# Optimization experiments

Hardware: AMD Instinct MI355X
Metric: run time of the kernel (lower is better)

The kernel has to match this reference:

```python
import jax, jax.numpy as jnp
import numpy as np

D_MODEL = 1024
N_HEADS = 16
D_HEAD = D_MODEL // N_HEADS  # 64
M = int(round(D_HEAD * np.log(D_HEAD)))  # 266 random features, per source
KERNEL_EPS = 1e-4


def setup_inputs() -> dict:
    key = jax.random.key(0)
    ks = jax.random.split(key, 12)
    B, L = 2, 2048
    sc = 1.0 / np.sqrt(D_MODEL)
    return {
        "query": jax.random.normal(ks[0], (B, L, D_MODEL), jnp.float32),
        "key_": jax.random.normal(ks[1], (B, L, D_MODEL), jnp.float32),
        "value": jax.random.normal(ks[2], (B, L, D_MODEL), jnp.float32),
        "Wq": jax.random.normal(ks[3], (D_MODEL, D_MODEL), jnp.float32) * sc,
        "bq": jnp.zeros((D_MODEL,), jnp.float32),
        "Wk": jax.random.normal(ks[4], (D_MODEL, D_MODEL), jnp.float32) * sc,
        "bk": jnp.zeros((D_MODEL,), jnp.float32),
        "Wv": jax.random.normal(ks[5], (D_MODEL, D_MODEL), jnp.float32) * sc,
        "bv": jnp.zeros((D_MODEL,), jnp.float32),
        "Wo": jax.random.normal(ks[6], (D_MODEL, D_MODEL), jnp.float32) * sc,
        "bo": jnp.zeros((D_MODEL,), jnp.float32),
        "random_features": jax.random.normal(ks[7], (M, D_HEAD), jnp.float32),
    }


def _split_heads(x):
    # [B,L,d_model] -> [B,H,L,D]
    B, L, _ = x.shape
    return x.reshape(B, L, N_HEADS, D_HEAD).transpose(0, 2, 1, 3)


def _favor_projected(q, k, rf):
    # q,k: [B,H,L,D]; rf: [M,D]. Faithful to get_projected_queries_and_keys (kernel_type='exp').
    q = q / (D_MODEL ** 0.25)
    k = k / (D_MODEL ** 0.25)
    pq = jnp.einsum('bhld,md->bhlm', q, rf)
    pk = jnp.einsum('bhld,md->bhlm', k, rf)
    h_q = -0.5 * jnp.sum(q * q, axis=-1, keepdims=True)  # [B,H,L,1]
    h_k = -0.5 * jnp.sum(k * k, axis=-1, keepdims=True)
    q_stab = jnp.max(h_q, axis=-1, keepdims=True)  # == h_q (last dim is 1), as in source
    k_stab = jnp.max(h_k)  # global scalar, as in source
    q_ker = jnp.exp(h_q + (pq - q_stab))
    k_ker = jnp.exp(h_k + (pk - k_stab))
    c = M ** (-0.5)
    return c * (q_ker + KERNEL_EPS), c * (k_ker + KERNEL_EPS)


def _causal_favor(qp, kp, v):
    # qp,kp: [L,B,H,M]; v: [L,B,H,D]. Prefix-sum linear attention.
    # Denominator: q_prime[i] . cumsum(k_prime)[i]
    denom = jnp.einsum('lbhm,lbhm->lbh', qp, jnp.cumsum(kp, axis=0))

    # Numerator: recurrent scan carrying S = sum_j k'_j v_j^T  ([B,H,M,D])
    def step(S, inp):
        q_t, k_t, v_t = inp
        S = S + k_t[..., :, None] * v_t[..., None, :]
        out_t = jnp.einsum('bhmd,bhm->bhd', S, q_t)
        return S, out_t

    S0 = jnp.zeros(kp.shape[1:] + (v.shape[-1],), kp.dtype)
    _, num = jax.lax.scan(step, S0, (qp, kp, v))  # num: [L,B,H,D]
    return num / denom[..., None]


def reference(query, key_, value, Wq, bq, Wk, bk, Wv, bv, Wo, bo, random_features):
    B, L, _ = query.shape
    q = _split_heads(query @ Wq + bq)   # [B,H,L,D]
    k = _split_heads(key_ @ Wk + bk)
    v = _split_heads(value @ Wv + bv)
    q_prime, k_prime = _favor_projected(q, k, random_features)  # [B,H,L,M]
    # Causal path operates sequence-first: [L,B,H,*]
    qp = q_prime.transpose(2, 0, 1, 3)
    kp = k_prime.transpose(2, 0, 1, 3)
    vt = v.transpose(2, 0, 1, 3)
    out = _causal_favor(qp, kp, vt)               # [L,B,H,D]
    ctx = out.transpose(1, 0, 2, 3).reshape(B, L, D_MODEL)
    return ctx @ Wo + bo
```

## Files before the change

kernel.cpp:

```cpp
#include <hip/hip_runtime.h>
#include <hip/hip_bf16.h>

#define BATCH 2
#define SEQ 2048
#define DMODEL 1024
#define NH 16
#define HD 64
#define NRF 266
#define NRFP 288
#define SROW 320
#define CHK 128
#define NCH 16
#define NBH 32
#define NROWS 4096

constexpr float SCAL = 0.17677669529663687f;
constexpr float SCAL2 = 0.03125f;
constexpr float LN_CNORM = -2.7917480361965505f;
constexpr float CKEPS = 6.131393094576169e-6f;

typedef short bf16x8 __attribute__((ext_vector_type(8)));
typedef float f32x4 __attribute__((ext_vector_type(4)));

__device__ __forceinline__ short f2bs(float v) {
  __hip_bfloat16 h = __float2bfloat16(v);
  return *reinterpret_cast<short*>(&h);
}
__device__ __forceinline__ float bs2f(short s) {
  __hip_bfloat16 h;
  *reinterpret_cast<short*>(&h) = s;
  return __bfloat162float(h);
}
__device__ __forceinline__ void gload_lds16(const void* g, void* l) {
  __builtin_amdgcn_global_load_lds(
      (const __attribute__((address_space(1))) void*)g,
      (__attribute__((address_space(3))) void*)l, 16, 0, 0);
}
__device__ __forceinline__ unsigned f2ord(float f) {
  unsigned u = __float_as_uint(f);
  return (u & 0x80000000u) ? ~u : (u | 0x80000000u);
}
__device__ __forceinline__ float ord2f(unsigned e) {
  return (e & 0x80000000u) ? __uint_as_float(e & 0x7fffffffu)
                           : __uint_as_float(~e);
}

__global__ __launch_bounds__(256) void cvt3_kernel(const float* __restrict__ q,
                                                   const float* __restrict__ k,
                                                   const float* __restrict__ v,
                                                   short* __restrict__ out) {
  int z = blockIdx.y;
  const float* x = (z == 0) ? q : (z == 1) ? k : v;
  short* y = out + (size_t)z * NROWS * DMODEL;
  int i = (blockIdx.x * 256 + threadIdx.x) * 8;
  float4 a = *(const float4*)&x[i];
  float4 b = *(const float4*)&x[i + 4];
  bf16x8 o;
  o[0] = f2bs(a.x); o[1] = f2bs(a.y); o[2] = f2bs(a.z); o[3] = f2bs(a.w);
  o[4] = f2bs(b.x); o[5] = f2bs(b.y); o[6] = f2bs(b.z); o[7] = f2bs(b.w);
  *(bf16x8*)&y[i] = o;
}

__global__ __launch_bounds__(256) void rf_pad_bf16(const float* __restrict__ rf,
                                                   short* __restrict__ rfb,
                                                   unsigned* __restrict__ kord) {
  int idx = blockIdx.x * 256 + threadIdx.x;
  rfb[idx] = (idx < NRF * HD) ? f2bs(rf[idx] * SCAL) : (short)0;
  if (idx == 0) *kord = 0u;
}

__global__ __launch_bounds__(256) void transpose4_bf16(
    const float* __restrict__ Wq, const float* __restrict__ Wk,
    const float* __restrict__ Wv, const float* __restrict__ Wo,
    short* __restrict__ WtBase) {
  __shared__ float t[32][33];
  int z = blockIdx.z;
  const float* W = (z == 0) ? Wq : (z == 1) ? Wk : (z == 2) ? Wv : Wo;
  short* Wt = WtBase + (size_t)z * DMODEL * DMODEL;
  int k0 = blockIdx.y << 5, n0 = blockIdx.x << 5;
  int tx = threadIdx.x & 31, ty = threadIdx.x >> 5;
#pragma unroll
  for (int rr = 0; rr < 4; ++rr) {
    int r = ty + (rr << 3);
    t[r][tx] = W[(size_t)(k0 + r) * DMODEL + n0 + tx];
  }
  __syncthreads();
#pragma unroll
  for (int rr = 0; rr < 4; ++rr) {
    int r = ty + (rr << 3);
    Wt[(size_t)(n0 + r) * DMODEL + k0 + tx] = f2bs(t[tx][r]);
  }
}

template <bool OUTBF>
__device__ __forceinline__ void gemm_core128(const short* __restrict__ A,
                                             const short* __restrict__ Bt,
                                             const float* __restrict__ bias,
                                             void* __restrict__ C, int bm, int bn) {
  __shared__ short As[2][128 * 64];
  __shared__ short Bs[2][128 * 64];
  int tid = threadIdx.x;
  int lane = tid & 63, wid = tid >> 6;
  int wr = wid >> 1, wc = wid & 1;
  int cl = lane & 15, rq = lane >> 4;
  f32x4 acc[4][4];
#pragma unroll
  for (int m = 0; m < 4; ++m)
#pragma unroll
    for (int n = 0; n < 4; ++n) acc[m][n] = f32x4{0.f, 0.f, 0.f, 0.f};

  auto stage = [&](int buf, int k0) {
#pragma unroll
    for (int i = 0; i < 4; ++i) {
      int e = tid * 8 + i * 2048;
      int row = e >> 6;
      int k = (e & 63) ^ ((row & 7) << 3);
      gload_lds16(A + (size_t)(bm + row) * DMODEL + k0 + k,
                  &As[buf][wid * 512 + i * 2048]);
    }
#pragma unroll
    for (int i = 0; i < 4; ++i) {
      int e = tid * 8 + i * 2048;
      int row = e >> 6;
      int k = (e & 63) ^ ((row & 7) << 3);
      gload_lds16(Bt + (size_t)(bn + row) * DMODEL + k0 + k,
                  &Bs[buf][wid * 512 + i * 2048]);
    }
  };

  stage(0, 0);
#pragma unroll 2
  for (int t = 0; t < 16; ++t) {
    int cur = t & 1;
    if (t < 15) {
      stage(cur ^ 1, (t + 1) * 64);
      asm volatile("s_waitcnt vmcnt(8)" ::: "memory");
    } else {
      asm volatile("s_waitcnt vmcnt(0)" ::: "memory");
    }
    __builtin_amdgcn_s_barrier();
    asm volatile("" ::: "memory");
    const short* curA = &As[cur][0];
    const short* curB = &Bs[cur][0];
#pragma unroll
    for (int ks = 0; ks < 2; ++ks) {
      int kb = ks * 32 + (rq << 3);
      bf16x8 af[4], bfv[4];
#pragma unroll
      for (int mf = 0; mf < 4; ++mf) {
        int row = wr * 64 + mf * 16 + cl;
        af[mf] = *(const bf16x8*)&curA[row * 64 + (kb ^ ((row & 7) << 3))];
      }
#pragma unroll
      for (int nf = 0; nf < 4; ++nf) {
        int row = wc * 64 + nf * 16 + cl;
        bfv[nf] = *(const bf16x8*)&curB[row * 64 + (kb ^ ((row & 7) << 3))];
      }
#pragma unroll
      for (int mf = 0; mf < 4; ++mf)
#pragma unroll
        for (int nf = 0; nf < 4; ++nf)
          acc[mf][nf] = __builtin_amdgcn_mfma_f32_16x16x32_bf16(af[mf], bfv[nf],
                                                                acc[mf][nf], 0, 0, 0);
    }
    __builtin_amdgcn_s_barrier();
    asm volatile("" ::: "memory");
  }
  int rbase = bm + wr * 64 + (rq << 2);
  int cbase = bn + wc * 64 + cl;
#pragma unroll
  for (int nf = 0; nf < 4; ++nf) {
    int col = cbase + nf * 16;
    float bv = bias[col];
#pragma unroll
    for (int mf = 0; mf < 4; ++mf)
#pragma unroll
      for (int r = 0; r < 4; ++r) {
        int row = rbase + mf * 16 + r;
        float v = acc[mf][nf][r] + bv;
        if (OUTBF)
          ((short*)C)[(size_t)row * DMODEL + col] = f2bs(v);
        else
          ((float*)C)[(size_t)row * DMODEL + col] = v;
      }
  }
}

template <bool OUTBF>
__device__ __forceinline__ void gemm_core64(const short* __restrict__ A,
                                            const short* __restrict__ Bt,
                                            const float* __restrict__ bias,
                                            void* __restrict__ C, int bm, int bn) {
  __shared__ short As[2][128 * 64];
  __shared__ short Bs[2][64 * 64];
  int tid = threadIdx.x;
  int lane = tid & 63, wid = tid >> 6;
  int wr = wid >> 1, wc = wid & 1;
  f32x4 acc[4][2];
#pragma unroll
  for (int m = 0; m < 4; ++m)
#pragma unroll
    for (int n = 0; n < 2; ++n) acc[m][n] = f32x4{0.f, 0.f, 0.f, 0.f};

  auto stage = [&](int buf, int k0) {
#pragma unroll
    for (int i = 0; i < 4; ++i) {
      int e = tid * 8 + i * 2048;
      int row = e >> 6;
      int k = (e & 63) ^ ((row & 7) << 3);
      gload_lds16(A + (size_t)(bm + row) * DMODEL + k0 + k,
                  &As[buf][wid * 512 + i * 2048]);
    }
#pragma unroll
    for (int i = 0; i < 2; ++i) {
      int e = tid * 8 + i * 2048;
      int row = e >> 6;
      int k = (e & 63) ^ ((row & 7) << 3);
      gload_lds16(Bt + (size_t)(bn + row) * DMODEL + k0 + k,
                  &Bs[buf][wid * 512 + i * 2048]);
    }
  };

  stage(0, 0);
#pragma unroll 2
  for (int t = 0; t < 16; ++t) {
    int cur = t & 1;
    if (t < 15) {
      stage(cur ^ 1, (t + 1) * 64);
      asm volatile("s_waitcnt vmcnt(6)" ::: "memory");
    } else {
      asm volatile("s_waitcnt vmcnt(0)" ::: "memory");
    }
    __builtin_amdgcn_s_barrier();
    asm volatile("" ::: "memory");
    const short* curA = &As[cur][0];
    const short* curB = &Bs[cur][0];
#pragma unroll
    for (int ks = 0; ks < 2; ++ks) {
      int kb = ks * 32 + ((lane >> 4) << 3);
      bf16x8 af[4], bfv[2];
#pragma unroll
      for (int mf = 0; mf < 4; ++mf) {
        int row = wr * 64 + mf * 16 + (lane & 15);
        af[mf] = *(const bf16x8*)&curA[row * 64 + (kb ^ ((row & 7) << 3))];
      }
#pragma unroll
      for (int nf = 0; nf < 2; ++nf) {
        int row = wc * 32 + nf * 16 + (lane & 15);
        bfv[nf] = *(const bf16x8*)&curB[row * 64 + (kb ^ ((row & 7) << 3))];
      }
#pragma unroll
      for (int mf = 0; mf < 4; ++mf)
#pragma unroll
        for (int nf = 0; nf < 2; ++nf)
          acc[mf][nf] = __builtin_amdgcn_mfma_f32_16x16x32_bf16(af[mf], bfv[nf],
                                                                acc[mf][nf], 0, 0, 0);
    }
    __builtin_amdgcn_s_barrier();
    asm volatile("" ::: "memory");
  }
  int rbase = bm + wr * 64 + ((lane >> 4) << 2);
  int cbase = bn + wc * 32 + (lane & 15);
#pragma unroll
  for (int nf = 0; nf < 2; ++nf) {
    int col = cbase + nf * 16;
    float bv = bias[col];
#pragma unroll
    for (int mf = 0; mf < 4; ++mf)
#pragma unroll
      for (int r = 0; r < 4; ++r) {
        int row = rbase + mf * 16 + r;
        float v = acc[mf][nf][r] + bv;
        if (OUTBF)
          ((short*)C)[(size_t)row * DMODEL + col] = f2bs(v);
        else
          ((float*)C)[(size_t)row * DMODEL + col] = v;
      }
  }
}

__global__ __launch_bounds__(256) void gemm_qkv3(
    const short* __restrict__ Abase, const short* __restrict__ WtBase,
    const float* __restrict__ bq, const float* __restrict__ bk,
    const float* __restrict__ bv, short* __restrict__ OutBase) {
  int z = blockIdx.z;
  const short* A = Abase + (size_t)z * NROWS * DMODEL;
  const short* Bt = WtBase + (size_t)z * DMODEL * DMODEL;
  const float* bias = (z == 0) ? bq : (z == 1) ? bk : bv;
  short* C = OutBase + (size_t)z * NROWS * DMODEL;
  int bid = blockIdx.x + (blockIdx.y << 3);
  int swz = ((bid & 7) << 5) + (bid >> 3);
  int bn = (swz & 7) << 7;
  int bm = (swz >> 3) << 7;
  gemm_core128<true>(A, Bt, bias, C, bm, bn);
}

__global__ __launch_bounds__(256) void gemm_out(const short* __restrict__ A,
                                                const short* __restrict__ Bt,
                                                const float* __restrict__ bias,
                                                float* __restrict__ C) {
  int bid = blockIdx.x + (blockIdx.y << 4);
  int swz = ((bid & 7) << 6) + (bid >> 3);
  int bn = (swz & 15) << 6;
  int bm = (swz >> 4) << 7;
  gemm_core64<false>(A, Bt, bias, C, bm, bn);
}

__global__ __launch_bounds__(256) void hk_kernel(const short* __restrict__ Kb,
                                                 float* __restrict__ hkbuf,
                                                 unsigned* __restrict__ kord) {
  int tid = threadIdx.x;
  int rloc = tid >> 4, h = tid & 15;
  int n = blockIdx.x * 16 + rloc;
  const short* p = Kb + (size_t)n * DMODEL + h * HD;
  float ss = 0.f;
#pragma unroll
  for (int g = 0; g < 8; ++g) {
    bf16x8 v = *(const bf16x8*)(p + g * 8);
#pragma unroll
    for (int e = 0; e < 8; ++e) {
      float x = bs2f(v[e]);
      ss += x * x;
    }
  }
  float hkv = -0.5f * SCAL2 * ss;
  int b = n >> 11, l = n & (SEQ - 1);
  hkbuf[((size_t)(b * NH + h)) * SEQ + l] = hkv;
  __shared__ float red[256];
  red[tid] = hkv;
  __syncthreads();
  for (int s = 128; s > 0; s >>= 1) {
    if (tid < s) red[tid] = fmaxf(red[tid], red[tid + s]);
    __syncthreads();
  }
  if (tid == 0) atomicMax(kord, f2ord(red[0]));
}

__global__ __launch_bounds__(256, 1) void featmap_mfma(
    const short* __restrict__ Qproj, const short* __restrict__ Kproj,
    const short* __restrict__ rfb, const float* __restrict__ hkbuf,
    const unsigned* __restrict__ kord, short* __restrict__ Qp,
    short* __restrict__ Kp) {
  __shared__ short smem[26624];
  __shared__ float hks[128];
  short* As = smem;
  short* Bs = smem + 8192;
  int isK = blockIdx.z;
  const short* X = isK ? Kproj : Qproj;
  short* O = isK ? Kp : Qp;
  int bh = blockIdx.y, b = bh >> 4, h = bh & 15;
  int l0 = blockIdx.x << 7;
  int tid = threadIdx.x, lane = tid & 63, wid = tid >> 6;
  int cl = lane & 15, rq = lane >> 4;

#pragma unroll
  for (int i = 0; i < 4; ++i) {
    int e = tid * 8 + i * 2048;
    int row = e >> 6;
    int k = (e & 63) ^ ((row & 7) << 3);
    gload_lds16(X + ((size_t)b * SEQ + l0 + row) * DMODEL + h * HD + k,
                &As[wid * 512 + i * 2048]);
  }
#pragma unroll
  for (int i = 0; i < 9; ++i) {
    int e = tid * 8 + i * 2048;
    int row = e >> 6;
    int k = (e & 63) ^ ((row & 7) << 3);
    gload_lds16(rfb + row * HD + k, &Bs[wid * 512 + i * 2048]);
  }
  if (isK) {
    float ksv = ord2f(*kord);
    if (tid < 128)
      hks[tid] = hkbuf[(size_t)bh * SEQ + l0 + tid] - ksv + LN_CNORM;
  }
  __syncthreads();

  int i0 = wid * 32;
  f32x4 acc[2][18];
#pragma unroll
  for (int m = 0; m < 2; ++m)
#pragma unroll
    for (int n = 0; n < 18; ++n) acc[m][n] = f32x4{0.f, 0.f, 0.f, 0.f};
#pragma unroll
  for (int ks = 0; ks < 2; ++ks) {
    int kb = ks * 32 + (rq << 3);
    int swz = (cl & 7) << 3;
    bf16x8 af[2];
#pragma unroll
    for (int mf = 0; mf < 2; ++mf) {
      int row = i0 + mf * 16 + cl;
      af[mf] = *(const bf16x8*)&As[row * 64 + (kb ^ swz)];
    }
#pragma unroll
    for (int nf = 0; nf < 18; ++nf) {
      int brow = nf * 16 + cl;
      bf16x8 bv = *(const bf16x8*)&Bs[brow * 64 + (kb ^ swz)];
#pragma unroll
      for (int mf = 0; mf < 2; ++mf)
        acc[mf][nf] = __builtin_amdgcn_mfma_f32_16x16x32_bf16(af[mf], bv,
                                                              acc[mf][nf], 0, 0, 0);
    }
  }

  short* Ps = smem;
#pragma unroll
  for (int hf = 0; hf < 2; ++hf) {
    __syncthreads();
#pragma unroll
    for (int mf = 0; mf < 2; ++mf)
#pragma unroll
      for (int r = 0; r < 4; ++r) {
        int rl = i0 + mf * 16 + (rq << 2) + r;
        float addk = isK ? hks[rl] : LN_CNORM;
#pragma unroll
        for (int nf2 = 0; nf2 < 9; ++nf2) {
          int m = hf * 144 + nf2 * 16 + cl;
          float v = acc[mf][hf * 9 + nf2][r] + addk;
          float o = (m < NRF) ? (__expf(v) + CKEPS) : 0.f;
          Ps[rl * 152 + nf2 * 16 + cl] = f2bs(o);
        }
      }
    __syncthreads();
#pragma unroll
    for (int it = 0; it < 9; ++it) {
      int idx = tid + it * 256;
      int row = idx / 18, ch = idx - row * 18;
      bf16x8 val = *(const bf16x8*)&Ps[row * 152 + ch * 8];
      *(bf16x8*)&O[((size_t)bh * SEQ + l0 + row) * NRFP + hf * 144 + ch * 8] = val;
    }
  }
}

__global__ __launch_bounds__(256) void chunksum_mfma(
    const short* __restrict__ Kp, const short* __restrict__ Vb,
    short* __restrict__ Sct, float* __restrict__ ksum) {
  constexpr int ST = 70;
  __shared__ short KT[NRFP * ST];
  __shared__ short VT[HD * ST];
  int c = blockIdx.x, bh = blockIdx.y;
  int b = bh >> 4, h = bh & 15;
  int tid = threadIdx.x, lane = tid & 63, wv = tid >> 6;
  int cl = lane & 15, rq = lane >> 4;
  int irow = tid >> 2;
  int mq = tid & 3;
  size_t rowb = (size_t)bh * SEQ + (size_t)c * CHK;

  f32x4 acc[18];
#pragma unroll
  for (int m = 0; m < 18; ++m) acc[m] = f32x4{0.f, 0.f, 0.f, 0.f};
  float k1 = 0.f, k2 = 0.f;

  for (int hf = 0; hf < 2; ++hf) {
    __syncthreads();
    const short* Krow = Kp + (rowb + hf * 64 + irow) * NRFP;
#pragma unroll
    for (int cg = 0; cg < 9; ++cg) {
      int m0 = cg * 32 + mq * 8;
      bf16x8 v = *(const bf16x8*)(Krow + m0);
#pragma unroll
      for (int e = 0; e < 8; ++e) KT[(m0 + e) * ST + irow] = v[e];
    }
    const short* Vrow =
        Vb + ((size_t)b * SEQ + (size_t)c * CHK + hf * 64 + irow) * DMODEL + h * HD;
    {
      int d0 = mq * 16;
      bf16x8 v0 = *(const bf16x8*)(Vrow + d0);
      bf16x8 v1 = *(const bf16x8*)(Vrow + d0 + 8);
#pragma unroll
      for (int e = 0; e < 8; ++e) VT[(d0 + e) * ST + irow] = v0[e];
#pragma unroll
      for (int e = 0; e < 8; ++e) VT[(d0 + 8 + e) * ST + irow] = v1[e];
    }
    __syncthreads();
#pragma unroll
    for (int ks = 0; ks < 2; ++ks) {
      int kb = ks * 32 + rq * 8;
      bf16x8 bv = *(const bf16x8*)&VT[(wv * 16 + cl) * ST + kb];
#pragma unroll
      for (int mf = 0; mf < 18; ++mf) {
        bf16x8 av = *(const bf16x8*)&KT[(mf * 16 + cl) * ST + kb];
        acc[mf] = __builtin_amdgcn_mfma_f32_16x16x32_bf16(av, bv, acc[mf], 0, 0, 0);
      }
    }
    {
      const short* r1 = &KT[tid * ST];
#pragma unroll
      for (int g = 0; g < 8; ++g) {
        bf16x8 v = *(const bf16x8*)(r1 + g * 8);
#pragma unroll
        for (int e = 0; e < 8; ++e) k1 += bs2f(v[e]);
      }
      if (tid < 10) {
        const short* r2 = &KT[(256 + tid) * ST];
#pragma unroll
        for (int g = 0; g < 8; ++g) {
          bf16x8 v = *(const bf16x8*)(r2 + g * 8);
#pragma unroll
          for (int e = 0; e < 8; ++e) k2 += bs2f(v[e]);
        }
      }
    }
  }
  size_t sbase = ((size_t)bh * NCH + c) * (size_t)(HD * SROW);
  int d = wv * 16 + cl;
#pragma unroll
  for (int mf = 0; mf < 18; ++mf) {
    short4 o4 = make_short4(f2bs(acc[mf][0]), f2bs(acc[mf][1]),
                            f2bs(acc[mf][2]), f2bs(acc[mf][3]));
    *(short4*)&Sct[sbase + (size_t)d * SROW + mf * 16 + rq * 4] = o4;
  }
  {
    int dz = tid >> 2, off = NRFP + ((tid & 3) << 3);
    bf16x8 z = {0, 0, 0, 0, 0, 0, 0, 0};
    *(bf16x8*)&Sct[sbase + (size_t)dz * SROW + off] = z;
  }
  size_t kbase = ((size_t)bh * NCH + c) * (size_t)NRF;
  if (tid < NRF) ksum[kbase + tid] = k1;
  if (tid < 10) ksum[kbase + 256 + tid] = k2;
}

__global__ __launch_bounds__(256) void prefix_all(const short* __restrict__ Sct,
                                                  short* __restrict__ Spt,
                                                  const float* __restrict__ ksum,
                                                  short* __restrict__ ksb) {
  int bh = blockIdx.y;
  if (blockIdx.x == 80) {
    for (int m = threadIdx.x; m < NRFP; m += 256) {
      if (m < NRF) {
        size_t base = (size_t)bh * NCH * NRF + m;
        float a = 0.f;
#pragma unroll
        for (int c = 0; c < NCH; ++c) {
          float v = ksum[base + (size_t)c * NRF];
          ksb[((size_t)bh * NCH + c) * NRFP + m] = f2bs(a);
          a += v;
        }
      } else {
#pragma unroll
        for (int c = 0; c < NCH; ++c)
          ksb[((size_t)bh * NCH + c) * NRFP + m] = 0;
      }
    }
    return;
  }
  int e = blockIdx.x * 256 + threadIdx.x;
  float a = 0.f;
#pragma unroll
  for (int c = 0; c < NCH; ++c) {
    size_t idx = ((size_t)bh * NCH + c) * (size_t)(HD * SROW) + e;
    float v = bs2f(Sct[idx]);
    Spt[idx] = f2bs(a);
    a += v;
  }
}

__global__ __launch_bounds__(256) void attn_mfma(
    const short* __restrict__ Qp, const short* __restrict__ Kp,
    const short* __restrict__ Vb, const short* __restrict__ Spt,
    const short* __restrict__ ksb, short* __restrict__ ctxb) {
  constexpr int PST = 136;
  __shared__ short Vt[64 * PST];
  __shared__ short SP[64 * SROW];
  __shared__ short Kb2[2][128 * 32];
  int c = blockIdx.x, bh = blockIdx.y;
  int b = bh >> 4, h = bh & 15;
  int tid = threadIdx.x, lane = tid & 63, wid = tid >> 6;
  int cl = lane & 15, rq = lane >> 4;
  size_t rowb = (size_t)bh * SEQ + (size_t)c * CHK;

  {
    int jj = tid >> 3, d0 = (tid & 7) << 3;
#pragma unroll
    for (int jt = 0; jt < 4; ++jt) {
      int j = jj + jt * 32;
      bf16x8 v = *(const bf16x8*)(Vb + ((size_t)b * SEQ + (size_t)c * CHK + j) * DMODEL +
                                  h * HD + d0);
#pragma unroll
      for (int e = 0; e < 8; ++e) Vt[(d0 + e) * PST + j] = v[e];
    }
  }
  const short* sg = Spt + ((size_t)bh * NCH + c) * (size_t)(HD * SROW);
#pragma unroll
  for (int i = 0; i < 10; ++i) {
    int o = tid * 8 + i * 2048;
    int d = o / SROW;
    int m = o - d * SROW;
    int ms = m ^ ((d & 7) << 3);
    gload_lds16(sg + (size_t)d * SROW + ms, &SP[wid * 512 + i * 2048]);
  }
  const short* Kbase = Kp + rowb * NRFP;
  auto stageK = [&](int buf, int k0) {
#pragma unroll
    for (int i = 0; i < 2; ++i) {
      int chunk = tid + i * 256;
      int row = chunk >> 2, cc = chunk & 3;
      int col = k0 + ((cc ^ (row & 3)) << 3);
      gload_lds16(Kbase + (size_t)row * NRFP + col,
                  &Kb2[buf][(wid * 64 + i * 256) * 8]);
    }
  };
  stageK(0, 0);

  int i0 = wid * 32;
  const short* Arow = Qp + (rowb + i0) * NRFP;
  const short* krow = ksb + ((size_t)bh * NCH + c) * NRFP;
  f32x4 accI[2][4];
  f32x4 accD[2];
  f32x4 accP[2][8];
#pragma unroll
  for (int m = 0; m < 2; ++m) {
#pragma unroll
    for (int n = 0; n < 4; ++n) accI[m][n] = f32x4{0.f, 0.f, 0.f, 0.f};
    accD[m] = f32x4{0.f, 0.f, 0.f, 0.f};
#pragma unroll
    for (int n = 0; n < 8; ++n) accP[m][n] = f32x4{0.f, 0.f, 0.f, 0.f};
  }
  for (int k9 = 0; k9 < 9; ++k9) {
    int cur = k9 & 1;
    if (k9 < 8) {
      stageK(cur ^ 1, (k9 + 1) * 32);
      asm volatile("s_waitcnt vmcnt(2)" ::: "memory");
    } else {
      asm volatile("s_waitcnt vmcnt(0)" ::: "memory");
    }
    __builtin_amdgcn_s_barrier();
    asm volatile("" ::: "memory");
    int kb = k9 * 32 + (rq << 3);
    bf16x8 af[2];
#pragma unroll
    for (int mf = 0; mf < 2; ++mf)
      af[mf] = *(const bf16x8*)(Arow + (size_t)(mf * 16 + cl) * NRFP + kb);
    bf16x8 bvD = {0, 0, 0, 0, 0, 0, 0, 0};
    if (cl == 0) bvD = *(const bf16x8*)(krow + kb);
#pragma unroll
    for (int mf = 0; mf < 2; ++mf)
      accD[mf] = __builtin_amdgcn_mfma_f32_16x16x32_bf16(af[mf], bvD, accD[mf], 0, 0, 0);
#pragma unroll
    for (int nf = 0; nf < 4; ++nf) {
      int row = nf * 16 + cl;
      bf16x8 bv = *(const bf16x8*)&SP[row * SROW + (kb ^ ((cl & 7) << 3))];
#pragma unroll
      for (int mf = 0; mf < 2; ++mf)
        accI[mf][nf] = __builtin_amdgcn_mfma_f32_16x16x32_bf16(af[mf], bv,
                                                               accI[mf][nf], 0, 0, 0);
    }
    const short* kcur = &Kb2[cur][0];
#pragma unroll
    for (int nf = 0; nf < 8; ++nf) {
      int row = nf * 16 + cl;
      bf16x8 bv = *(const bf16x8*)&kcur[row * 32 + ((rq ^ (cl & 3)) << 3)];
#pragma unroll
      for (int mf = 0; mf < 2; ++mf)
        accP[mf][nf] = __builtin_amdgcn_mfma_f32_16x16x32_bf16(af[mf], bv,
                                                               accP[mf][nf], 0, 0, 0);
    }
    __builtin_amdgcn_s_barrier();
    asm volatile("" ::: "memory");
  }

  float dtot[2][4];
#pragma unroll
  for (int mf = 0; mf < 2; ++mf)
#pragma unroll
    for (int r = 0; r < 4; ++r) {
      int rl = mf * 16 + (rq << 2) + r;
      int row = i0 + rl;
      float dsum = 0.f;
#pragma unroll
      for (int nf = 0; nf < 8; ++nf) {
        int col = nf * 16 + cl;
        float v = (col > row) ? 0.f : accP[mf][nf][r];
        dsum += v;
        SP[wid * 32 * PST + rl * PST + col] = f2bs(v);
      }
      dsum += __shfl_xor(dsum, 1);
      dsum += __shfl_xor(dsum, 2);
      dsum += __shfl_xor(dsum, 4);
      dsum += __shfl_xor(dsum, 8);
      float dden = __shfl(accD[mf][r], lane & 48);
      dtot[mf][r] = dden + dsum;
    }
  __syncthreads();

  f32x4 pacc[2][4];
#pragma unroll
  for (int m = 0; m < 2; ++m)
#pragma unroll
    for (int n = 0; n < 4; ++n) pacc[m][n] = f32x4{0.f, 0.f, 0.f, 0.f};
#pragma unroll
  for (int kk = 0; kk < 4; ++kk) {
    int kb = kk * 32 + (rq << 3);
    bf16x8 paf[2];
#pragma unroll
    for (int mf = 0; mf < 2; ++mf)
      paf[mf] = *(const bf16x8*)&SP[wid * 32 * PST + (mf * 16 + cl) * PST + kb];
#pragma unroll
    for (int nf = 0; nf < 4; ++nf) {
      bf16x8 bv = *(const bf16x8*)&Vt[(nf * 16 + cl) * PST + kb];
#pragma unroll
      for (int mf = 0; mf < 2; ++mf)
        pacc[mf][nf] = __builtin_amdgcn_mfma_f32_16x16x32_bf16(paf[mf], bv,
                                                               pacc[mf][nf], 0, 0, 0);
    }
  }
#pragma unroll
  for (int mf = 0; mf < 2; ++mf)
#pragma unroll
    for (int r = 0; r < 4; ++r) {
      int row = i0 + mf * 16 + (rq << 2) + r;
      float inv = 1.0f / dtot[mf][r];
      size_t ob = ((size_t)b * SEQ + (size_t)c * CHK + row) * DMODEL + h * HD;
#pragma unroll
      for (int nf = 0; nf < 4; ++nf) {
        int d = nf * 16 + cl;
        float v = (accI[mf][nf][r] + pacc[mf][nf][r]) * inv;
        ctxb[ob + d] = f2bs(v);
      }
    }
}

extern "C" void kernel_launch(void* const* d_in, const int* in_sizes, int n_in,
                              void* d_out, int out_size, void* d_ws, size_t ws_size,
                              hipStream_t stream) {
  (void)in_sizes; (void)n_in; (void)out_size;
  const float* query = (const float*)d_in[0];
  const float* key_  = (const float*)d_in[1];
  const float* value = (const float*)d_in[2];
  const float* Wq = (const float*)d_in[3];
  const float* bq = (const float*)d_in[4];
  const float* Wk = (const float*)d_in[5];
  const float* bk = (const float*)d_in[6];
  const float* Wv = (const float*)d_in[7];
  const float* bv = (const float*)d_in[8];
  const float* Wo = (const float*)d_in[9];
  const float* bo = (const float*)d_in[10];
  const float* rf = (const float*)d_in[11];

  constexpr size_t SZ_INBF = (size_t)NROWS * DMODEL * 2;
  constexpr size_t SZ_QP   = (size_t)NBH * SEQ * NRFP * 2;
  constexpr size_t SZ_WT   = (size_t)DMODEL * DMODEL * 2;
  constexpr size_t SZ_SCH  = (size_t)NBH * NCH * HD * SROW * 2;
  constexpr size_t SZ_KS   = (size_t)NBH * NCH * NRF * 4;
  constexpr size_t SZ_KSB  = (size_t)NBH * NCH * NRFP * 2;
  constexpr size_t SZ_HK   = (size_t)NBH * SEQ * 4;
  constexpr size_t SZ_RFB  = (size_t)NRFP * HD * 2;

  constexpr size_t O_QP   = 0;
  constexpr size_t O_KP   = O_QP + SZ_QP;
  constexpr size_t O_WT   = O_KP + SZ_QP;
  constexpr size_t O_QPR  = O_WT + 4 * SZ_WT;
  constexpr size_t O_SCH  = O_QPR + 3 * SZ_INBF;
  constexpr size_t O_SPR  = O_SCH + SZ_SCH;
  constexpr size_t O_KSUM = O_SPR + SZ_SCH;
  constexpr size_t O_KSB  = O_KSUM + SZ_KS;
  constexpr size_t O_HK   = O_KSB + SZ_KSB;
  constexpr size_t O_KST  = O_HK + SZ_HK;
  constexpr size_t O_CTXB = O_KST + 256;
  constexpr size_t O_RFB  = O_CTXB + SZ_INBF;
  constexpr size_t O_END  = O_RFB + SZ_RFB;
  if (ws_size < O_END) return;

  char* w = (char*)d_ws;
  short* Qbf  = (short*)(w + O_QP);
  short* Qp   = (short*)(w + O_QP);
  short* Kp   = (short*)(w + O_KP);
  short* WtB  = (short*)(w + O_WT);
  short* QprB = (short*)(w + O_QPR);
  short* Kpr  = (short*)(w + O_QPR + SZ_INBF);
  short* Vpr  = (short*)(w + O_QPR + 2 * SZ_INBF);
  short* Sct  = (short*)(w + O_SCH);
  short* Spt  = (short*)(w + O_SPR);
  float* ksum = (float*)(w + O_KSUM);
  short* ksb  = (short*)(w + O_KSB);
  float* hkbuf = (float*)(w + O_HK);
  unsigned* kord = (unsigned*)(w + O_KST);
  short* ctxb = (short*)(w + O_CTXB);
  short* rfb  = (short*)(w + O_RFB);

  constexpr int NEL = NROWS * DMODEL;
  cvt3_kernel<<<dim3(NEL / 2048, 3), 256, 0, stream>>>(query, key_, value, Qbf);
  transpose4_bf16<<<dim3(32, 32, 4), 256, 0, stream>>>(Wq, Wk, Wv, Wo, WtB);
  rf_pad_bf16<<<(NRFP * HD) / 256, 256, 0, stream>>>(rf, rfb, kord);
  gemm_qkv3<<<dim3(8, 32, 3), 256, 0, stream>>>(Qbf, WtB, bq, bk, bv, QprB);
  hk_kernel<<<256, 256, 0, stream>>>(Kpr, hkbuf, kord);
  featmap_mfma<<<dim3(SEQ / 128, NBH, 2), 256, 0, stream>>>(QprB, Kpr, rfb, hkbuf,
                                                            kord, Qp, Kp);
  chunksum_mfma<<<dim3(NCH, NBH), 256, 0, stream>>>(Kp, Vpr, Sct, ksum);
  prefix_all<<<dim3(81, NBH), 256, 0, stream>>>(Sct, Spt, ksum, ksb);
  attn_mfma<<<dim3(NCH, NBH), 256, 0, stream>>>(Qp, Kp, Vpr, Spt, ksb, ctxb);
  gemm_out<<<dim3(16, 32), 256, 0, stream>>>(ctxb, WtB + 3 * (size_t)DMODEL * DMODEL,
                                             bo, (float*)d_out);
}
```

Before: 171.3 us.

## Fuse key-norm computation into featmap, drop global stabilizer, merge rf padding

Measured after the change: 164.3 us. -4.1%, faster.

```diff
diff --git a/kernel.cpp b/kernel.cpp
--- a/kernel.cpp
+++ b/kernel.cpp
@@ -35,14 +35,6 @@
   __builtin_amdgcn_global_load_lds(
       (const __attribute__((address_space(1))) void*)g,
       (__attribute__((address_space(3))) void*)l, 16, 0, 0);
-}
-__device__ __forceinline__ unsigned f2ord(float f) {
-  unsigned u = __float_as_uint(f);
-  return (u & 0x80000000u) ? ~u : (u | 0x80000000u);
-}
-__device__ __forceinline__ float ord2f(unsigned e) {
-  return (e & 0x80000000u) ? __uint_as_float(e & 0x7fffffffu)
-                           : __uint_as_float(~e);
 }
 
 __global__ __launch_bounds__(256) void cvt3_kernel(const float* __restrict__ q,
@@ -61,20 +53,19 @@
   *(bf16x8*)&y[i] = o;
 }
 
-__global__ __launch_bounds__(256) void rf_pad_bf16(const float* __restrict__ rf,
-                                                   short* __restrict__ rfb,
-                                                   unsigned* __restrict__ kord) {
-  int idx = blockIdx.x * 256 + threadIdx.x;
-  rfb[idx] = (idx < NRF * HD) ? f2bs(rf[idx] * SCAL) : (short)0;
-  if (idx == 0) *kord = 0u;
-}
-
-__global__ __launch_bounds__(256) void transpose4_bf16(
+__global__ __launch_bounds__(256) void transpose5_bf16(
     const float* __restrict__ Wq, const float* __restrict__ Wk,
     const float* __restrict__ Wv, const float* __restrict__ Wo,
-    short* __restrict__ WtBase) {
+    const float* __restrict__ rf, short* __restrict__ WtBase,
+    short* __restrict__ rfb) {
+  int z = blockIdx.z;
+  if (z == 4) {
+    int idx = (blockIdx.y * 32 + blockIdx.x) * 256 + threadIdx.x;
+    if (idx < NRFP * HD)
+      rfb[idx] = (idx < NRF * HD) ? f2bs(rf[idx] * SCAL) : (short)0;
+    return;
+  }
   __shared__ float t[32][33];
-  int z = blockIdx.z;
   const float* W = (z == 0) ? Wq : (z == 1) ? Wk : (z == 2) ? Wv : Wo;
   short* Wt = WtBase + (size_t)z * DMODEL * DMODEL;
   int k0 = blockIdx.y << 5, n0 = blockIdx.x << 5;
@@ -109,23 +100,22 @@
 #pragma unroll
     for (int n = 0; n < 4; ++n) acc[m][n] = f32x4{0.f, 0.f, 0.f, 0.f};
 
+  size_t abase[4], bbase[4];
+#pragma unroll
+  for (int i = 0; i < 4; ++i) {
+    int e = tid * 8 + i * 2048;
+    int row = e >> 6;
+    int k = (e & 63) ^ ((row & 7) << 3);
+    abase[i] = (size_t)(bm + row) * DMODEL + k;
+    bbase[i] = (size_t)(bn + row) * DMODEL + k;
+  }
   auto stage = [&](int buf, int k0) {
 #pragma unroll
-    for (int i = 0; i < 4; ++i) {
-      int e = tid * 8 + i * 2048;
-      int row = e >> 6;
-      int k = (e & 63) ^ ((row & 7) << 3);
-      gload_lds16(A + (size_t)(bm + row) * DMODEL + k0 + k,
-                  &As[buf][wid * 512 + i * 2048]);
-    }
-#pragma unroll
-    for (int i = 0; i < 4; ++i) {
-      int e = tid * 8 + i * 2048;
-      int row = e >> 6;
-      int k = (e & 63) ^ ((row & 7) << 3);
-      gload_lds16(Bt + (size_t)(bn + row) * DMODEL + k0 + k,
-                  &Bs[buf][wid * 512 + i * 2048]);
-    }
+    for (int i = 0; i < 4; ++i)
+      gload_lds16(A + abase[i] + k0, &As[buf][wid * 512 + i * 2048]);
+#pragma unroll
+    for (int i = 0; i < 4; ++i)
+      gload_lds16(Bt + bbase[i] + k0, &Bs[buf][wid * 512 + i * 2048]);
   };
 
   stage(0, 0);
@@ -202,23 +192,22 @@
 #pragma unroll
     for (int n = 0; n < 2; ++n) acc[m][n] = f32x4{0.f, 0.f, 0.f, 0.f};
 
+  size_t abase[4], bbase[2];
+#pragma unroll
+  for (int i = 0; i < 4; ++i) {
+    int e = tid * 8 + i * 2048;
+    int row = e >> 6;
+    int k = (e & 63) ^ ((row & 7) << 3);
+    abase[i] = (size_t)(bm + row) * DMODEL + k;
+    if (i < 2) bbase[i] = (size_t)(bn + row) * DMODEL + k;
+  }
   auto stage = [&](int buf, int k0) {
 #pragma unroll
-    for (int i = 0; i < 4; ++i) {
-      int e = tid * 8 + i * 2048;
-      int row = e >> 6;
-      int k = (e & 63) ^ ((row & 7) << 3);
-      gload_lds16(A + (size_t)(bm + row) * DMODEL + k0 + k,
-                  &As[buf][wid * 512 + i * 2048]);
-    }
-#pragma unroll
-    for (int i = 0; i < 2; ++i) {
-      int e = tid * 8 + i * 2048;
-      int row = e >> 6;
-      int k = (e & 63) ^ ((row & 7) << 3);
-      gload_lds16(Bt + (size_t)(bn + row) * DMODEL + k0 + k,
-                  &Bs[buf][wid * 512 + i * 2048]);
-    }
+    for (int i = 0; i < 4; ++i)
+      gload_lds16(A + abase[i] + k0, &As[buf][wid * 512 + i * 2048]);
+#pragma unroll
+    for (int i = 0; i < 2; ++i)
+      gload_lds16(Bt + bbase[i] + k0, &Bs[buf][wid * 512 + i * 2048]);
   };
 
   stage(0, 0);
@@ -306,41 +295,9 @@
   gemm_core64<false>(A, Bt, bias, C, bm, bn);
 }
 
-__global__ __launch_bounds__(256) void hk_kernel(const short* __restrict__ Kb,
-                                                 float* __restrict__ hkbuf,
-                                                 unsigned* __restrict__ kord) {
-  int tid = threadIdx.x;
-  int rloc = tid >> 4, h = tid & 15;
-  int n = blockIdx.x * 16 + rloc;
-  const short* p = Kb + (size_t)n * DMODEL + h * HD;
-  float ss = 0.f;
-#pragma unroll
-  for (int g = 0; g < 8; ++g) {
-    bf16x8 v = *(const bf16x8*)(p + g * 8);
-#pragma unroll
-    for (int e = 0; e < 8; ++e) {
-      float x = bs2f(v[e]);
-      ss += x * x;
-    }
-  }
-  float hkv = -0.5f * SCAL2 * ss;
-  int b = n >> 11, l = n & (SEQ - 1);
-  hkbuf[((size_t)(b * NH + h)) * SEQ + l] = hkv;
-  __shared__ float red[256];
-  red[tid] = hkv;
-  __syncthreads();
-  for (int s = 128; s > 0; s >>= 1) {
-    if (tid < s) red[tid] = fmaxf(red[tid], red[tid + s]);
-    __syncthreads();
-  }
-  if (tid == 0) atomicMax(kord, f2ord(red[0]));
-}
-
 __global__ __launch_bounds__(256, 1) void featmap_mfma(
     const short* __restrict__ Qproj, const short* __restrict__ Kproj,
-    const short* __restrict__ rfb, const float* __restrict__ hkbuf,
-    const unsigned* __restrict__ kord, short* __restrict__ Qp,
-    short* __restrict__ Kp) {
+    const short* __restrict__ rfb, short* __restrict__ Qp, short* __restrict__ Kp) {
   __shared__ short smem[26624];
   __shared__ float hks[128];
   short* As = smem;
@@ -368,11 +325,6 @@
     int k = (e & 63) ^ ((row & 7) << 3);
     gload_lds16(rfb + row * HD + k, &Bs[wid * 512 + i * 2048]);
   }
-  if (isK) {
-    float ksv = ord2f(*kord);
-    if (tid < 128)
-      hks[tid] = hkbuf[(size_t)bh * SEQ + l0 + tid] - ksv + LN_CNORM;
-  }
   __syncthreads();
 
   int i0 = wid * 32;
@@ -400,6 +352,23 @@
         acc[mf][nf] = __builtin_amdgcn_mfma_f32_16x16x32_bf16(af[mf], bv,
                                                               acc[mf][nf], 0, 0, 0);
     }
+  }
+
+  if (isK) {
+    int row = tid >> 1, half = tid & 1;
+    const short* rp = &As[row * 64 + half * 32];
+    float ss = 0.f;
+#pragma unroll
+    for (int g = 0; g < 4; ++g) {
+      bf16x8 v = *(const bf16x8*)(rp + g * 8);
+#pragma unroll
+      for (int e = 0; e < 8; ++e) {
+        float x = bs2f(v[e]);
+        ss += x * x;
+      }
+    }
+    ss += __shfl_xor(ss, 1);
+    if (!half) hks[row] = -0.5f * SCAL2 * ss + LN_CNORM;
   }
 
   short* Ps = smem;
@@ -742,7 +711,6 @@
   constexpr size_t SZ_SCH  = (size_t)NBH * NCH * HD * SROW * 2;
   constexpr size_t SZ_KS   = (size_t)NBH * NCH * NRF * 4;
   constexpr size_t SZ_KSB  = (size_t)NBH * NCH * NRFP * 2;
-  constexpr size_t SZ_HK   = (size_t)NBH * SEQ * 4;
   constexpr size_t SZ_RFB  = (size_t)NRFP * HD * 2;
 
   constexpr size_t O_QP   = 0;
@@ -753,9 +721,7 @@
   constexpr size_t O_SPR  = O_SCH + SZ_SCH;
   constexpr size_t O_KSUM = O_SPR + SZ_SCH;
   constexpr size_t O_KSB  = O_KSUM + SZ_KS;
-  constexpr size_t O_HK   = O_KSB + SZ_KSB;
-  constexpr size_t O_KST  = O_HK + SZ_HK;
-  constexpr size_t O_CTXB = O_KST + 256;
+  constexpr size_t O_CTXB = O_KSB + SZ_KSB;
   constexpr size_t O_RFB  = O_CTXB + SZ_INBF;
   constexpr size_t O_END  = O_RFB + SZ_RFB;
   if (ws_size < O_END) return;
@@ -772,19 +738,14 @@
   short* Spt  = (short*)(w + O_SPR);
   float* ksum = (float*)(w + O_KSUM);
   short* ksb  = (short*)(w + O_KSB);
-  float* hkbuf = (float*)(w + O_HK);
-  unsigned* kord = (unsigned*)(w + O_KST);
   short* ctxb = (short*)(w + O_CTXB);
   short* rfb  = (short*)(w + O_RFB);
 
   constexpr int NEL = NROWS * DMODEL;
   cvt3_kernel<<<dim3(NEL / 2048, 3), 256, 0, stream>>>(query, key_, value, Qbf);
-  transpose4_bf16<<<dim3(32, 32, 4), 256, 0, stream>>>(Wq, Wk, Wv, Wo, WtB);
-  rf_pad_bf16<<<(NRFP * HD) / 256, 256, 0, stream>>>(rf, rfb, kord);
+  transpose5_bf16<<<dim3(32, 32, 5), 256, 0, stream>>>(Wq, Wk, Wv, Wo, rf, WtB, rfb);
   gemm_qkv3<<<dim3(8, 32, 3), 256, 0, stream>>>(Qbf, WtB, bq, bk, bv, QprB);
-  hk_kernel<<<256, 256, 0, stream>>>(Kpr, hkbuf, kord);
-  featmap_mfma<<<dim3(SEQ / 128, NBH, 2), 256, 0, stream>>>(QprB, Kpr, rfb, hkbuf,
-                                                            kord, Qp, Kp);
+  featmap_mfma<<<dim3(SEQ / 128, NBH, 2), 256, 0, stream>>>(QprB, Kpr, rfb, Qp, Kp);
   chunksum_mfma<<<dim3(NCH, NBH), 256, 0, stream>>>(Kp, Vpr, Sct, ksum);
   prefix_all<<<dim3(81, NBH), 256, 0, stream>>>(Sct, Spt, ksum, ksb);
   attn_mfma<<<dim3(NCH, NBH), 256, 0, stream>>>(Qp, Kp, Vpr, Spt, ksb, ctxb);
```
